# Optimization experiments

Measured on AMD Instinct MI355X. Metric: run time of the kernel, lower is better.

Reference implementation:

```python
import jax, jax.numpy as jnp
import numpy as np

B, N, DM, H, C, DC = 4, 1024, 512, 8, 3, 16  # batch, nodes, node_dim, heads, manifold components, per-component dim
DK = DM // H


def setup_inputs() -> dict:
    key = jax.random.key(0)
    ks = jax.random.split(key, 8)

    def lin_w(k):
        return jax.random.normal(k, (DM, DM), jnp.float32) / np.sqrt(DM).astype(np.float32)

    return {
        "h": jax.random.normal(ks[0], (B, N, DM), jnp.float32),
        "x": jax.random.normal(ks[1], (B, N, C * DC), jnp.float32),
        "Wq": lin_w(ks[2]), "bq": jnp.zeros((DM,), jnp.float32),
        "Wk": lin_w(ks[3]), "bk": jnp.zeros((DM,), jnp.float32),
        "Wv": lin_w(ks[4]), "bv": jnp.zeros((DM,), jnp.float32),
        "Wo": lin_w(ks[5]), "bo": jnp.zeros((DM,), jnp.float32),
        "alpha": jnp.ones((H, C), jnp.float32),
        "log_sigma": jnp.zeros((H, C), jnp.float32),
    }


def reference(h, x, Wq, bq, Wk, bk, Wv, bv, Wo, bo, alpha, log_sigma):
    b, n, dm = h.shape
    hh, cc = alpha.shape
    dk = dm // hh
    scale = 1.0 / np.sqrt(dk).astype(np.float32)

    def to_heads(t, W, bias):
        return (t @ W.T + bias).reshape(b, n, hh, dk).transpose(0, 2, 1, 3)  # (B,H,N,dk)

    Q = to_heads(h, Wq, bq)
    K = to_heads(h, Wk, bk)
    V = to_heads(h, Wv, bv)

    attn = jnp.einsum('bhid,bhjd->bhij', Q, K) * scale  # (B,H,N,N)

    # Geodesic kernel: per-component Euclidean distances on the product manifold.
    xs = x.reshape(b, n, cc, -1)                      # (B,N,C,dc)
    sq = jnp.sum(xs * xs, axis=-1)                    # (B,N,C)
    inner = jnp.einsum('bicd,bjcd->bijc', xs, xs)     # (B,N,N,C)
    d_sq = jnp.maximum(sq[:, :, None, :] + sq[:, None, :, :] - 2.0 * inner, 0.0)  # (B,N,N,C)

    sigma = jnp.clip(jnp.exp(log_sigma), 1e-4)        # (H,C)
    # exp(-d_c^2 / (2 sigma_{h,c}^2)) -> (B,H,N,N,C), then weight by alpha and sum over c
    e = jnp.exp(-d_sq[:, None] / (2.0 * (sigma ** 2)[None, :, None, None, :])).astype(attn.dtype)
    attn = attn + jnp.einsum('hc,bhijc->bhij', alpha, e)

    p = jax.nn.softmax(attn, axis=-1)
    out = jnp.einsum('bhij,bhjd->bhid', p, V)         # (B,H,N,dk)
    out = out.transpose(0, 2, 1, 3).reshape(b, n, dm)
    return out @ Wo.T + bo
```

## Files before the change

### kernel.cpp

```cpp
#include <hip/hip_runtime.h>

typedef __bf16 bf16;
typedef __attribute__((ext_vector_type(8))) __bf16 bf16x8;
typedef __attribute__((ext_vector_type(4))) float f32x4;

#define LOG2E 1.44269504088896f
#define SCALE 0.125f

__device__ inline f32x4 mfma16(bf16x8 a, bf16x8 b, f32x4 c) {
    return __builtin_amdgcn_mfma_f32_16x16x32_bf16(a, b, c, 0, 0, 0);
}

__global__ __launch_bounds__(256) void prep_kernel(
        const float* __restrict__ h, const float* __restrict__ x,
        const float* __restrict__ Wq, const float* __restrict__ Wk,
        const float* __restrict__ Wv, const float* __restrict__ Wo,
        const float* __restrict__ bq, const float* __restrict__ bk,
        const float* __restrict__ bv,
        bf16* __restrict__ hb, bf16* __restrict__ wpack, bf16* __restrict__ wob,
        float* __restrict__ bqkv, bf16* __restrict__ xb, float* __restrict__ sqx) {
    int stride = gridDim.x * blockDim.x;
    int tid = blockIdx.x * blockDim.x + threadIdx.x;
    for (int i = tid; i < 4096 * 512; i += stride) hb[i] = (bf16)h[i];
    for (int i = tid; i < 3 * 512 * 512; i += stride) {
        float v = (i < 262144) ? Wq[i] : (i < 524288 ? Wk[i - 262144] : Wv[i - 524288]);
        wpack[i] = (bf16)v;
    }
    for (int i = tid; i < 512 * 512; i += stride) wob[i] = (bf16)Wo[i];
    for (int i = tid; i < 1536; i += stride)
        bqkv[i] = (i < 512) ? bq[i] : (i < 1024 ? bk[i - 512] : bv[i - 1024]);
    for (int i = tid; i < 4096 * 48; i += stride) xb[i] = (bf16)x[i];
    for (int i = tid; i < 4096 * 3; i += stride) {
        int row = i / 3, c = i - row * 3;
        float s = 0.0f;
        for (int k = 0; k < 16; k++) {
            float v = (float)(bf16)x[row * 48 + c * 16 + k];
            s += v * v;
        }
        sqx[i] = s;
    }
}

__global__ __launch_bounds__(256) void gemm_qkv_kernel(
        const bf16* __restrict__ A, const bf16* __restrict__ Bm,
        const float* __restrict__ bias,
        bf16* __restrict__ Qb, bf16* __restrict__ Kb, bf16* __restrict__ Vt) {
    __shared__ bf16 Al[64][72];
    __shared__ bf16 Bl[64][72];
    int t = threadIdx.x;
    int w = t >> 6, lane = t & 63, g = lane >> 4, lo = lane & 15;
    int rowbase = blockIdx.x * 64, colbase = blockIdx.y * 64;
    int wr = (w >> 1) * 32, wc = (w & 1) * 32;
    f32x4 acc[2][2] = {};
    int sr = t >> 2, sc = (t & 3) * 16;
    for (int kb = 0; kb < 512; kb += 64) {
        *(bf16x8*)&Al[sr][sc]     = *(const bf16x8*)&A[(rowbase + sr) * 512 + kb + sc];
        *(bf16x8*)&Al[sr][sc + 8] = *(const bf16x8*)&A[(rowbase + sr) * 512 + kb + sc + 8];
        *(bf16x8*)&Bl[sr][sc]     = *(const bf16x8*)&Bm[(colbase + sr) * 512 + kb + sc];
        *(bf16x8*)&Bl[sr][sc + 8] = *(const bf16x8*)&Bm[(colbase + sr) * 512 + kb + sc + 8];
        __syncthreads();
        for (int kk = 0; kk < 64; kk += 32) {
            bf16x8 af[2], bfr[2];
            af[0]  = *(const bf16x8*)&Al[wr + lo][kk + 8 * g];
            af[1]  = *(const bf16x8*)&Al[wr + 16 + lo][kk + 8 * g];
            bfr[0] = *(const bf16x8*)&Bl[wc + lo][kk + 8 * g];
            bfr[1] = *(const bf16x8*)&Bl[wc + 16 + lo][kk + 8 * g];
            for (int ri = 0; ri < 2; ri++)
                for (int ci = 0; ci < 2; ci++)
                    acc[ri][ci] = mfma16(af[ri], bfr[ci], acc[ri][ci]);
        }
        __syncthreads();
    }
    for (int ri = 0; ri < 2; ri++)
        for (int ci = 0; ci < 2; ci++) {
            int mcol = colbase + wc + 16 * ci + lo;
            float bv = bias[mcol];
            int proj = mcol >> 9, hm = mcol & 511, head = hm >> 6, d = hm & 63;
            for (int r = 0; r < 4; r++) {
                int n = rowbase + wr + 16 * ri + 4 * g + r;
                int bidx = n >> 10, i = n & 1023;
                bf16 val = (bf16)(acc[ri][ci][r] + bv);
                if (proj == 0)
                    Qb[((size_t)(bidx * 8 + head) * 1024 + i) * 64 + d] = val;
                else if (proj == 1)
                    Kb[((size_t)(bidx * 8 + head) * 1024 + i) * 64 + d] = val;
                else
                    Vt[((size_t)(bidx * 8 + head) * 64 + d) * 1024 + i] = val;
            }
        }
}

__global__ __launch_bounds__(256) void attn_kernel(
        const bf16* __restrict__ Qb, const bf16* __restrict__ Kb,
        const bf16* __restrict__ Vt, const bf16* __restrict__ xb,
        const float* __restrict__ sqx, const float* __restrict__ alpha,
        const float* __restrict__ log_sigma, int nsplit,
        float* __restrict__ o_part, float* __restrict__ ml_part) {
    __shared__ bf16 Klds[64][72];
    __shared__ bf16 Xlds[64][56];
    __shared__ bf16 VTlds[64][72];
    __shared__ float sqj[3][64];
    __shared__ bf16 Plds[4][16][72];

    int t = threadIdx.x;
    int w = t >> 6, lane = t & 63, g = lane >> 4, lo = lane & 15;
    int zz = blockIdx.z;
    int b = zz / nsplit, split = zz - b * nsplit;
    int hh = blockIdx.y;
    int i0 = blockIdx.x * 64 + w * 16;

    float alf[3], coef[3];
    for (int c = 0; c < 3; c++) {
        alf[c] = alpha[hh * 3 + c];
        float sg = expf(log_sigma[hh * 3 + c]);
        sg = fmaxf(sg, 1e-4f);
        coef[c] = -LOG2E / (2.0f * sg * sg);
    }

    const bf16* Qbase = Qb + ((size_t)(b * 8 + hh) * 1024 + i0) * 64;
    bf16x8 qa[2];
    qa[0] = *(const bf16x8*)&Qbase[lo * 64 + 8 * g];
    qa[1] = *(const bf16x8*)&Qbase[lo * 64 + 32 + 8 * g];

    bf16x8 xqa[3];
    const bf16* Xibase = xb + ((size_t)(b << 10) + i0) * 48;
    for (int c = 0; c < 3; c++) {
        bf16x8 v = {};
        if (g < 2) v = *(const bf16x8*)&Xibase[lo * 48 + c * 16 + 8 * g];
        xqa[c] = v;
    }

    float sqi[3][4];
    const float* sqibase = sqx + ((size_t)(b << 10) + i0) * 3;
    for (int r = 0; r < 4; r++)
        for (int c = 0; c < 3; c++) sqi[c][r] = sqibase[(4 * g + r) * 3 + c];

    float m_r[4], l_r[4];
    f32x4 o[4];
    for (int r = 0; r < 4; r++) { m_r[r] = -1e30f; l_r[r] = 0.0f; }
    for (int td = 0; td < 4; td++) o[td] = (f32x4){0.f, 0.f, 0.f, 0.f};

    int sr = t >> 2, sc = (t & 3) * 16;
    int jlen = 1024 / nsplit, jb = split * jlen;
    for (int j0 = jb; j0 < jb + jlen; j0 += 64) {
        __syncthreads();
        const bf16* Kbase = Kb + ((size_t)(b * 8 + hh) * 1024 + j0) * 64;
        *(bf16x8*)&Klds[sr][sc]     = *(const bf16x8*)&Kbase[sr * 64 + sc];
        *(bf16x8*)&Klds[sr][sc + 8] = *(const bf16x8*)&Kbase[sr * 64 + sc + 8];
        const bf16* Vbase = Vt + ((size_t)(b * 8 + hh) * 64) * 1024 + j0;
        *(bf16x8*)&VTlds[sr][sc]     = *(const bf16x8*)&Vbase[sr * 1024 + sc];
        *(bf16x8*)&VTlds[sr][sc + 8] = *(const bf16x8*)&Vbase[sr * 1024 + sc + 8];
        for (int idx = t; idx < 384; idx += 256) {
            int xr = idx / 6, xc = (idx - xr * 6) * 8;
            *(bf16x8*)&Xlds[xr][xc] = *(const bf16x8*)&xb[((size_t)(b << 10) + j0 + xr) * 48 + xc];
        }
        if (t < 192) {
            int jl = t / 3, c = t - jl * 3;
            sqj[c][jl] = sqx[((size_t)(b << 10) + j0 + jl) * 3 + c];
        }
        __syncthreads();

        f32x4 s[4];
        for (int tt = 0; tt < 4; tt++) {
            f32x4 acc = {};
            bf16x8 kb0 = *(const bf16x8*)&Klds[16 * tt + lo][8 * g];
            bf16x8 kb1 = *(const bf16x8*)&Klds[16 * tt + lo][32 + 8 * g];
            acc = mfma16(qa[0], kb0, acc);
            acc = mfma16(qa[1], kb1, acc);
            f32x4 ic[3];
            for (int c = 0; c < 3; c++) {
                bf16x8 xbf = {};
                if (g < 2) xbf = *(const bf16x8*)&Xlds[16 * tt + lo][c * 16 + 8 * g];
                f32x4 z = {};
                ic[c] = mfma16(xqa[c], xbf, z);
            }
            for (int r = 0; r < 4; r++) {
                float sv = acc[r] * SCALE;
                for (int c = 0; c < 3; c++) {
                    float d = sqi[c][r] + sqj[c][16 * tt + lo] - 2.0f * ic[c][r];
                    d = fmaxf(d, 0.0f);
                    sv += alf[c] * exp2f(coef[c] * d);
                }
                acc[r] = sv;
            }
            s[tt] = acc;
        }

        float pm[4], sf[4], rs[4];
        for (int r = 0; r < 4; r++)
            pm[r] = fmaxf(fmaxf(s[0][r], s[1][r]), fmaxf(s[2][r], s[3][r]));
        for (int msk = 1; msk < 16; msk <<= 1)
            for (int r = 0; r < 4; r++) pm[r] = fmaxf(pm[r], __shfl_xor(pm[r], msk));
        for (int r = 0; r < 4; r++) {
            float mn = fmaxf(m_r[r], pm[r]);
            sf[r] = exp2f((m_r[r] - mn) * LOG2E);
            m_r[r] = mn;
            rs[r] = 0.0f;
        }
        for (int tt = 0; tt < 4; tt++)
            for (int r = 0; r < 4; r++) {
                float p = exp2f((s[tt][r] - m_r[r]) * LOG2E);
                s[tt][r] = p;
                rs[r] += p;
            }
        for (int msk = 1; msk < 16; msk <<= 1)
            for (int r = 0; r < 4; r++) rs[r] += __shfl_xor(rs[r], msk);
        for (int r = 0; r < 4; r++) l_r[r] = l_r[r] * sf[r] + rs[r];

        for (int tt = 0; tt < 4; tt++)
            for (int r = 0; r < 4; r++)
                Plds[w][4 * g + r][16 * tt + lo] = (bf16)s[tt][r];

        for (int td = 0; td < 4; td++)
            for (int r = 0; r < 4; r++) o[td][r] *= sf[r];

        bf16x8 pa0 = *(const bf16x8*)&Plds[w][lo][8 * g];
        bf16x8 pa1 = *(const bf16x8*)&Plds[w][lo][32 + 8 * g];
        for (int td = 0; td < 4; td++) {
            bf16x8 vb0 = *(const bf16x8*)&VTlds[16 * td + lo][8 * g];
            bf16x8 vb1 = *(const bf16x8*)&VTlds[16 * td + lo][32 + 8 * g];
            o[td] = mfma16(pa0, vb0, o[td]);
            o[td] = mfma16(pa1, vb1, o[td]);
        }
    }

    for (int td = 0; td < 4; td++)
        for (int r = 0; r < 4; r++) {
            int i = i0 + 4 * g + r;
            size_t rowg = (size_t)(b * 8 + hh) * 1024 + i;
            o_part[((size_t)split * 32768 + rowg) * 64 + 16 * td + lo] = o[td][r];
        }
    if (lo == 0)
        for (int r = 0; r < 4; r++) {
            int i = i0 + 4 * g + r;
            size_t rowg = (size_t)(b * 8 + hh) * 1024 + i;
            ml_part[((size_t)split * 32768 + rowg) * 2]     = m_r[r];
            ml_part[((size_t)split * 32768 + rowg) * 2 + 1] = l_r[r];
        }
}

__global__ __launch_bounds__(256) void merge_kernel(
        const float* __restrict__ o_part, const float* __restrict__ ml_part,
        int nsplit, bf16* __restrict__ attnout) {
    int t = threadIdx.x;
    int rowg = blockIdx.x * 16 + (t >> 4);
    int d4 = (t & 15) * 4;
    float m0 = ml_part[(size_t)rowg * 2], l0 = ml_part[(size_t)rowg * 2 + 1];
    float m1 = -1e30f, l1 = 0.0f;
    if (nsplit == 2) {
        m1 = ml_part[((size_t)32768 + rowg) * 2];
        l1 = ml_part[((size_t)32768 + rowg) * 2 + 1];
    }
    float M = fmaxf(m0, m1);
    float w0 = exp2f((m0 - M) * LOG2E);
    float w1 = exp2f((m1 - M) * LOG2E);
    float inv = 1.0f / (w0 * l0 + w1 * l1);
    f32x4 a = *(const f32x4*)&o_part[(size_t)rowg * 64 + d4];
    f32x4 bv = (f32x4){0.f, 0.f, 0.f, 0.f};
    if (nsplit == 2) bv = *(const f32x4*)&o_part[((size_t)32768 + rowg) * 64 + d4];
    int b = rowg >> 13, hh = (rowg >> 10) & 7, i = rowg & 1023;
    bf16* dst = &attnout[((size_t)(b << 10) + i) * 512 + hh * 64 + d4];
    for (int q = 0; q < 4; q++)
        dst[q] = (bf16)((w0 * a[q] + w1 * bv[q]) * inv);
}

__global__ __launch_bounds__(256) void gemm_out_kernel(
        const bf16* __restrict__ A, const bf16* __restrict__ Bm,
        const float* __restrict__ bias, float* __restrict__ out) {
    __shared__ bf16 Al[64][72];
    __shared__ bf16 Bl[64][72];
    int t = threadIdx.x;
    int w = t >> 6, lane = t & 63, g = lane >> 4, lo = lane & 15;
    int rowbase = blockIdx.x * 64, colbase = blockIdx.y * 64;
    int wr = (w >> 1) * 32, wc = (w & 1) * 32;
    f32x4 acc[2][2] = {};
    int sr = t >> 2, sc = (t & 3) * 16;
    for (int kb = 0; kb < 512; kb += 64) {
        *(bf16x8*)&Al[sr][sc]     = *(const bf16x8*)&A[(rowbase + sr) * 512 + kb + sc];
        *(bf16x8*)&Al[sr][sc + 8] = *(const bf16x8*)&A[(rowbase + sr) * 512 + kb + sc + 8];
        *(bf16x8*)&Bl[sr][sc]     = *(const bf16x8*)&Bm[(colbase + sr) * 512 + kb + sc];
        *(bf16x8*)&Bl[sr][sc + 8] = *(const bf16x8*)&Bm[(colbase + sr) * 512 + kb + sc + 8];
        __syncthreads();
        for (int kk = 0; kk < 64; kk += 32) {
            bf16x8 af[2], bfr[2];
            af[0]  = *(const bf16x8*)&Al[wr + lo][kk + 8 * g];
            af[1]  = *(const bf16x8*)&Al[wr + 16 + lo][kk + 8 * g];
            bfr[0] = *(const bf16x8*)&Bl[wc + lo][kk + 8 * g];
            bfr[1] = *(const bf16x8*)&Bl[wc + 16 + lo][kk + 8 * g];
            for (int ri = 0; ri < 2; ri++)
                for (int ci = 0; ci < 2; ci++)
                    acc[ri][ci] = mfma16(af[ri], bfr[ci], acc[ri][ci]);
        }
        __syncthreads();
    }
    for (int ri = 0; ri < 2; ri++)
        for (int ci = 0; ci < 2; ci++) {
            int mcol = colbase + wc + 16 * ci + lo;
            float bv = bias[mcol];
            for (int r = 0; r < 4; r++) {
                int n = rowbase + wr + 16 * ri + 4 * g + r;
                out[(size_t)n * 512 + mcol] = acc[ri][ci][r] + bv;
            }
        }
}

extern "C" void kernel_launch(void* const* d_in, const int* in_sizes, int n_in,
                              void* d_out, int out_size, void* d_ws, size_t ws_size,
                              hipStream_t stream) {
    const float* h  = (const float*)d_in[0];
    const float* x  = (const float*)d_in[1];
    const float* Wq = (const float*)d_in[2];
    const float* bq = (const float*)d_in[3];
    const float* Wk = (const float*)d_in[4];
    const float* bk = (const float*)d_in[5];
    const float* Wv = (const float*)d_in[6];
    const float* bv = (const float*)d_in[7];
    const float* Wo = (const float*)d_in[8];
    const float* bo = (const float*)d_in[9];
    const float* alpha     = (const float*)d_in[10];
    const float* log_sigma = (const float*)d_in[11];
    float* out = (float*)d_out;

    char* ws = (char*)d_ws;
    size_t off = 0;
    auto alloc = [&](size_t bytes) {
        char* p = ws + off;
        off += (bytes + 255) & ~(size_t)255;
        return p;
    };
    bf16*  hb      = (bf16*)alloc(4096 * 512 * 2);
    bf16*  wpack   = (bf16*)alloc(1536 * 512 * 2);
    bf16*  wob     = (bf16*)alloc(512 * 512 * 2);
    float* bqkv    = (float*)alloc(1536 * 4);
    bf16*  xb      = (bf16*)alloc(4096 * 48 * 2);
    float* sqx     = (float*)alloc(4096 * 3 * 4);
    bf16*  Qb      = (bf16*)alloc((size_t)4 * 8 * 1024 * 64 * 2);
    bf16*  Kb      = (bf16*)alloc((size_t)4 * 8 * 1024 * 64 * 2);
    bf16*  Vt      = (bf16*)alloc((size_t)4 * 8 * 1024 * 64 * 2);
    bf16*  attnout = (bf16*)alloc(4096 * 512 * 2);
    size_t base = off;

    size_t need2 = base + 2 * ((size_t)32768 * 64 * 4 + 1024) + 2 * ((size_t)32768 * 2 * 4 + 1024);
    int nsplit = (ws_size >= need2) ? 2 : 1;
    float* o_part  = (float*)alloc((size_t)nsplit * 32768 * 64 * 4);
    float* ml_part = (float*)alloc((size_t)nsplit * 32768 * 2 * 4);

    prep_kernel<<<512, 256, 0, stream>>>(h, x, Wq, Wk, Wv, Wo, bq, bk, bv,
                                         hb, wpack, wob, bqkv, xb, sqx);
    gemm_qkv_kernel<<<dim3(64, 24), 256, 0, stream>>>(hb, wpack, bqkv, Qb, Kb, Vt);
    attn_kernel<<<dim3(16, 8, 4 * nsplit), 256, 0, stream>>>(
        Qb, Kb, Vt, xb, sqx, alpha, log_sigma, nsplit, o_part, ml_part);
    merge_kernel<<<2048, 256, 0, stream>>>(o_part, ml_part, nsplit, attnout);
    gemm_out_kernel<<<dim3(64, 8), 256, 0, stream>>>(attnout, wob, bo, out);
}
```

Baseline: 211.0 us.

## Factor Gaussian kernel into per-row and per-column exponentials and coalesce QKV stores

Rewrites exp(-(si+sj-2ij)/2σ²) as A_i·B_j·exp(ij/σ²), with the per-row and per-column factors (alpha folded into the row factor) computed once in the prep kernel. This cuts the inner-loop work to one exp and two FMAs per component and drops the clamp to zero. The QKV GEMM epilogue now stages its tile in LDS and writes coalesced 16-byte vectors, including a transposed write for V. The P buffer shares LDS with the X tile to reduce shared memory, at the cost of an extra barrier. Removing the clamp and factoring the exponential can overflow or underflow for large norms or small sigma, which is a numerical risk.

```diff
diff --git a/kernel.cpp b/kernel.cpp
--- a/kernel.cpp
+++ b/kernel.cpp
@@ -16,9 +16,11 @@
         const float* __restrict__ Wq, const float* __restrict__ Wk,
         const float* __restrict__ Wv, const float* __restrict__ Wo,
         const float* __restrict__ bq, const float* __restrict__ bk,
-        const float* __restrict__ bv,
+        const float* __restrict__ bv, const float* __restrict__ alpha,
+        const float* __restrict__ log_sigma,
         bf16* __restrict__ hb, bf16* __restrict__ wpack, bf16* __restrict__ wob,
-        float* __restrict__ bqkv, bf16* __restrict__ xb, float* __restrict__ sqx) {
+        float* __restrict__ bqkv, bf16* __restrict__ xb,
+        float* __restrict__ Aexp, float* __restrict__ Bexp) {
     int stride = gridDim.x * blockDim.x;
     int tid = blockIdx.x * blockDim.x + threadIdx.x;
     for (int i = tid; i < 4096 * 512; i += stride) hb[i] = (bf16)h[i];
@@ -37,7 +39,14 @@
             float v = (float)(bf16)x[row * 48 + c * 16 + k];
             s += v * v;
         }
-        sqx[i] = s;
+        int b = row >> 10, jj = row & 1023;
+        for (int hh = 0; hh < 8; hh++) {
+            float sg = fmaxf(expf(log_sigma[hh * 3 + c]), 1e-4f);
+            float coef = -(0.5f * LOG2E) / (sg * sg);
+            float e = exp2f(coef * s);
+            Aexp[((size_t)row * 8 + hh) * 3 + c] = alpha[hh * 3 + c] * e;
+            Bexp[(((size_t)(b * 8 + hh)) * 1024 + jj) * 3 + c] = e;
+        }
     }
 }
 
@@ -73,48 +82,54 @@
     }
     for (int ri = 0; ri < 2; ri++)
         for (int ci = 0; ci < 2; ci++) {
-            int mcol = colbase + wc + 16 * ci + lo;
-            float bv = bias[mcol];
-            int proj = mcol >> 9, hm = mcol & 511, head = hm >> 6, d = hm & 63;
-            for (int r = 0; r < 4; r++) {
-                int n = rowbase + wr + 16 * ri + 4 * g + r;
-                int bidx = n >> 10, i = n & 1023;
-                bf16 val = (bf16)(acc[ri][ci][r] + bv);
-                if (proj == 0)
-                    Qb[((size_t)(bidx * 8 + head) * 1024 + i) * 64 + d] = val;
-                else if (proj == 1)
-                    Kb[((size_t)(bidx * 8 + head) * 1024 + i) * 64 + d] = val;
-                else
-                    Vt[((size_t)(bidx * 8 + head) * 64 + d) * 1024 + i] = val;
-            }
-        }
+            int ccol = wc + 16 * ci + lo;
+            float bv = bias[colbase + ccol];
+            for (int r = 0; r < 4; r++)
+                Al[wr + 16 * ri + 4 * g + r][ccol] = (bf16)(acc[ri][ci][r] + bv);
+        }
+    __syncthreads();
+    int proj = colbase >> 9, head = (colbase >> 6) & 7;
+    int bidx = rowbase >> 10, i0 = rowbase & 1023;
+    int row = t >> 2, c16 = (t & 3) * 16;
+    if (proj < 2) {
+        bf16* dst = (proj == 0 ? Qb : Kb) +
+                    ((size_t)(bidx * 8 + head) * 1024 + i0 + row) * 64 + c16;
+        *(bf16x8*)dst       = *(const bf16x8*)&Al[row][c16];
+        *(bf16x8*)(dst + 8) = *(const bf16x8*)&Al[row][c16 + 8];
+    } else {
+        bf16x8 v0, v1;
+        for (int k = 0; k < 8; k++) v0[k] = Al[c16 + k][row];
+        for (int k = 0; k < 8; k++) v1[k] = Al[c16 + 8 + k][row];
+        bf16* dst = Vt + ((size_t)(bidx * 8 + head) * 64 + row) * 1024 + i0 + c16;
+        *(bf16x8*)dst       = v0;
+        *(bf16x8*)(dst + 8) = v1;
+    }
 }
 
 __global__ __launch_bounds__(256) void attn_kernel(
         const bf16* __restrict__ Qb, const bf16* __restrict__ Kb,
         const bf16* __restrict__ Vt, const bf16* __restrict__ xb,
-        const float* __restrict__ sqx, const float* __restrict__ alpha,
+        const float* __restrict__ Aexp, const float* __restrict__ Bexp,
         const float* __restrict__ log_sigma, int nsplit,
         float* __restrict__ o_part, float* __restrict__ ml_part) {
     __shared__ bf16 Klds[64][72];
-    __shared__ bf16 Xlds[64][56];
     __shared__ bf16 VTlds[64][72];
-    __shared__ float sqj[3][64];
-    __shared__ bf16 Plds[4][16][72];
+    __shared__ float Blds[3][64];
+    __shared__ __align__(16) char PXbuf[9216];
+    bf16 (*Xlds)[56] = (bf16 (*)[56])PXbuf;
 
     int t = threadIdx.x;
     int w = t >> 6, lane = t & 63, g = lane >> 4, lo = lane & 15;
+    bf16* Pw = (bf16*)PXbuf + (size_t)w * 16 * 72;
     int zz = blockIdx.z;
     int b = zz / nsplit, split = zz - b * nsplit;
     int hh = blockIdx.y;
     int i0 = blockIdx.x * 64 + w * 16;
 
-    float alf[3], coef[3];
+    float k2[3];
     for (int c = 0; c < 3; c++) {
-        alf[c] = alpha[hh * 3 + c];
-        float sg = expf(log_sigma[hh * 3 + c]);
-        sg = fmaxf(sg, 1e-4f);
-        coef[c] = -LOG2E / (2.0f * sg * sg);
+        float sg = fmaxf(expf(log_sigma[hh * 3 + c]), 1e-4f);
+        k2[c] = LOG2E / (sg * sg);
     }
 
     const bf16* Qbase = Qb + ((size_t)(b * 8 + hh) * 1024 + i0) * 64;
@@ -130,10 +145,10 @@
         xqa[c] = v;
     }
 
-    float sqi[3][4];
-    const float* sqibase = sqx + ((size_t)(b << 10) + i0) * 3;
+    float af[3][4];
     for (int r = 0; r < 4; r++)
-        for (int c = 0; c < 3; c++) sqi[c][r] = sqibase[(4 * g + r) * 3 + c];
+        for (int c = 0; c < 3; c++)
+            af[c][r] = Aexp[(((size_t)(b << 10) + i0 + 4 * g + r) * 8 + hh) * 3 + c];
 
     float m_r[4], l_r[4];
     f32x4 o[4];
@@ -155,8 +170,8 @@
             *(bf16x8*)&Xlds[xr][xc] = *(const bf16x8*)&xb[((size_t)(b << 10) + j0 + xr) * 48 + xc];
         }
         if (t < 192) {
-            int jl = t / 3, c = t - jl * 3;
-            sqj[c][jl] = sqx[((size_t)(b << 10) + j0 + jl) * 3 + c];
+            int jl = t & 63, c = t >> 6;
+            Blds[c][jl] = Bexp[(((size_t)(b * 8 + hh)) * 1024 + j0 + jl) * 3 + c];
         }
         __syncthreads();
 
@@ -174,17 +189,19 @@
                 f32x4 z = {};
                 ic[c] = mfma16(xqa[c], xbf, z);
             }
+            float B0 = Blds[0][16 * tt + lo];
+            float B1 = Blds[1][16 * tt + lo];
+            float B2 = Blds[2][16 * tt + lo];
             for (int r = 0; r < 4; r++) {
                 float sv = acc[r] * SCALE;
-                for (int c = 0; c < 3; c++) {
-                    float d = sqi[c][r] + sqj[c][16 * tt + lo] - 2.0f * ic[c][r];
-                    d = fmaxf(d, 0.0f);
-                    sv += alf[c] * exp2f(coef[c] * d);
-                }
+                sv = fmaf(af[0][r] * B0, exp2f(k2[0] * ic[0][r]), sv);
+                sv = fmaf(af[1][r] * B1, exp2f(k2[1] * ic[1][r]), sv);
+                sv = fmaf(af[2][r] * B2, exp2f(k2[2] * ic[2][r]), sv);
                 acc[r] = sv;
             }
             s[tt] = acc;
         }
+        __syncthreads();
 
         float pm[4], sf[4], rs[4];
         for (int r = 0; r < 4; r++)
@@ -209,13 +226,13 @@
 
         for (int tt = 0; tt < 4; tt++)
             for (int r = 0; r < 4; r++)
-                Plds[w][4 * g + r][16 * tt + lo] = (bf16)s[tt][r];
+                Pw[(4 * g + r) * 72 + 16 * tt + lo] = (bf16)s[tt][r];
 
         for (int td = 0; td < 4; td++)
             for (int r = 0; r < 4; r++) o[td][r] *= sf[r];
 
-        bf16x8 pa0 = *(const bf16x8*)&Plds[w][lo][8 * g];
-        bf16x8 pa1 = *(const bf16x8*)&Plds[w][lo][32 + 8 * g];
+        bf16x8 pa0 = *(const bf16x8*)&Pw[lo * 72 + 8 * g];
+        bf16x8 pa1 = *(const bf16x8*)&Pw[lo * 72 + 32 + 8 * g];
         for (int td = 0; td < 4; td++) {
             bf16x8 vb0 = *(const bf16x8*)&VTlds[16 * td + lo][8 * g];
             bf16x8 vb1 = *(const bf16x8*)&VTlds[16 * td + lo][32 + 8 * g];
@@ -333,7 +350,8 @@
     bf16*  wob     = (bf16*)alloc(512 * 512 * 2);
     float* bqkv    = (float*)alloc(1536 * 4);
     bf16*  xb      = (bf16*)alloc(4096 * 48 * 2);
-    float* sqx     = (float*)alloc(4096 * 3 * 4);
+    float* Aexp    = (float*)alloc((size_t)4096 * 8 * 3 * 4);
+    float* Bexp    = (float*)alloc((size_t)4096 * 8 * 3 * 4);
     bf16*  Qb      = (bf16*)alloc((size_t)4 * 8 * 1024 * 64 * 2);
     bf16*  Kb      = (bf16*)alloc((size_t)4 * 8 * 1024 * 64 * 2);
     bf16*  Vt      = (bf16*)alloc((size_t)4 * 8 * 1024 * 64 * 2);
@@ -346,10 +364,11 @@
     float* ml_part = (float*)alloc((size_t)nsplit * 32768 * 2 * 4);
 
     prep_kernel<<<512, 256, 0, stream>>>(h, x, Wq, Wk, Wv, Wo, bq, bk, bv,
-                                         hb, wpack, wob, bqkv, xb, sqx);
+                                         alpha, log_sigma,
+                                         hb, wpack, wob, bqkv, xb, Aexp, Bexp);
     gemm_qkv_kernel<<<dim3(64, 24), 256, 0, stream>>>(hb, wpack, bqkv, Qb, Kb, Vt);
     attn_kernel<<<dim3(16, 8, 4 * nsplit), 256, 0, stream>>>(
-        Qb, Kb, Vt, xb, sqx, alpha, log_sigma, nsplit, o_part, ml_part);
+        Qb, Kb, Vt, xb, Aexp, Bexp, log_sigma, nsplit, o_part, ml_part);
     merge_kernel<<<2048, 256, 0, stream>>>(o_part, ml_part, nsplit, attnout);
     gemm_out_kernel<<<dim3(64, 8), 256, 0, stream>>>(attnout, wob, bo, out);
 }
```

Result: faster. 200.8 us (-4.8%).

## Fold geodesic norms into MFMA, drop online softmax max, enlarge GEMM tiles

Applied to the files above, without the earlier changes.

The attention kernel now builds augmented x vectors in which -0.5*||x||^2 (split into bf16 hi/lo parts) and ones sit in padding lanes. A single MFMA per component then yields -d^2/2 directly, replacing the scalar per-element distance arithmetic. The online softmax max tracking, rescaling and cross-lane shuffles are removed: scores are exponentiated directly, and row sums come from an MFMA against a ones vector, which simplifies the merge kernel. This relies on scores staying small enough not to overflow fp32 exp2, so it is numerically less robust for general inputs. Both projection GEMMs move from 64x64 to 128x128 tiles, and the QKV GEMM stages its output through LDS so Q, K and transposed V stores are coalesced.

```diff
diff --git a/kernel.cpp b/kernel.cpp
--- a/kernel.cpp
+++ b/kernel.cpp
@@ -1,4 +1,5 @@
 #include <hip/hip_runtime.h>
+#include <math.h>
 
 typedef __bf16 bf16;
 typedef __attribute__((ext_vector_type(8))) __bf16 bf16x8;
@@ -9,6 +10,9 @@
 
 __device__ inline f32x4 mfma16(bf16x8 a, bf16x8 b, f32x4 c) {
     return __builtin_amdgcn_mfma_f32_16x16x32_bf16(a, b, c, 0, 0, 0);
+}
+__device__ inline unsigned short bfb(bf16 v) {
+    union { bf16 b; unsigned short u; } z; z.b = v; return z.u;
 }
 
 __global__ __launch_bounds__(256) void prep_kernel(
@@ -18,13 +22,15 @@
         const float* __restrict__ bq, const float* __restrict__ bk,
         const float* __restrict__ bv,
         bf16* __restrict__ hb, bf16* __restrict__ wpack, bf16* __restrict__ wob,
-        float* __restrict__ bqkv, bf16* __restrict__ xb, float* __restrict__ sqx) {
+        float* __restrict__ bqkv, bf16* __restrict__ xb,
+        unsigned* __restrict__ spack) {
     int stride = gridDim.x * blockDim.x;
     int tid = blockIdx.x * blockDim.x + threadIdx.x;
     for (int i = tid; i < 4096 * 512; i += stride) hb[i] = (bf16)h[i];
-    for (int i = tid; i < 3 * 512 * 512; i += stride) {
-        float v = (i < 262144) ? Wq[i] : (i < 524288 ? Wk[i - 262144] : Wv[i - 524288]);
-        wpack[i] = (bf16)v;
+    for (int i = tid; i < 262144; i += stride) {
+        wpack[i]          = (bf16)Wq[i];
+        wpack[262144 + i] = (bf16)Wk[i];
+        wpack[524288 + i] = (bf16)Wv[i];
     }
     for (int i = tid; i < 512 * 512; i += stride) wob[i] = (bf16)Wo[i];
     for (int i = tid; i < 1536; i += stride)
@@ -37,7 +43,10 @@
             float v = (float)(bf16)x[row * 48 + c * 16 + k];
             s += v * v;
         }
-        sqx[i] = s;
+        s = -0.5f * s;
+        bf16 sh = (bf16)s;
+        bf16 sl = (bf16)(s - (float)sh);
+        spack[i] = (unsigned)bfb(sh) | ((unsigned)bfb(sl) << 16);
     }
 }
 
@@ -45,61 +54,71 @@
         const bf16* __restrict__ A, const bf16* __restrict__ Bm,
         const float* __restrict__ bias,
         bf16* __restrict__ Qb, bf16* __restrict__ Kb, bf16* __restrict__ Vt) {
-    __shared__ bf16 Al[64][72];
-    __shared__ bf16 Bl[64][72];
-    int t = threadIdx.x;
-    int w = t >> 6, lane = t & 63, g = lane >> 4, lo = lane & 15;
-    int rowbase = blockIdx.x * 64, colbase = blockIdx.y * 64;
-    int wr = (w >> 1) * 32, wc = (w & 1) * 32;
-    f32x4 acc[2][2] = {};
-    int sr = t >> 2, sc = (t & 3) * 16;
+    __shared__ bf16 smem[2 * 128 * 72];
+    bf16 (*Asm)[72] = (bf16(*)[72])smem;
+    bf16 (*Bsm)[72] = (bf16(*)[72])(smem + 128 * 72);
+    int t = threadIdx.x, w = t >> 6, lane = t & 63, g = lane >> 4, lo = lane & 15;
+    int rowbase = blockIdx.x * 128, colbase = blockIdx.y * 128;
+    int wr = (w >> 1) * 64, wc = (w & 1) * 64;
+    f32x4 acc[4][4] = {};
+    int srow = t >> 2, scol = (t & 3) * 16;
     for (int kb = 0; kb < 512; kb += 64) {
-        *(bf16x8*)&Al[sr][sc]     = *(const bf16x8*)&A[(rowbase + sr) * 512 + kb + sc];
-        *(bf16x8*)&Al[sr][sc + 8] = *(const bf16x8*)&A[(rowbase + sr) * 512 + kb + sc + 8];
-        *(bf16x8*)&Bl[sr][sc]     = *(const bf16x8*)&Bm[(colbase + sr) * 512 + kb + sc];
-        *(bf16x8*)&Bl[sr][sc + 8] = *(const bf16x8*)&Bm[(colbase + sr) * 512 + kb + sc + 8];
+        __syncthreads();
+        for (int half = 0; half < 2; half++) {
+            int r = srow + 64 * half;
+            *(bf16x8*)&Asm[r][scol]     = *(const bf16x8*)&A[(size_t)(rowbase + r) * 512 + kb + scol];
+            *(bf16x8*)&Asm[r][scol + 8] = *(const bf16x8*)&A[(size_t)(rowbase + r) * 512 + kb + scol + 8];
+            *(bf16x8*)&Bsm[r][scol]     = *(const bf16x8*)&Bm[(size_t)(colbase + r) * 512 + kb + scol];
+            *(bf16x8*)&Bsm[r][scol + 8] = *(const bf16x8*)&Bm[(size_t)(colbase + r) * 512 + kb + scol + 8];
+        }
         __syncthreads();
         for (int kk = 0; kk < 64; kk += 32) {
-            bf16x8 af[2], bfr[2];
-            af[0]  = *(const bf16x8*)&Al[wr + lo][kk + 8 * g];
-            af[1]  = *(const bf16x8*)&Al[wr + 16 + lo][kk + 8 * g];
-            bfr[0] = *(const bf16x8*)&Bl[wc + lo][kk + 8 * g];
-            bfr[1] = *(const bf16x8*)&Bl[wc + 16 + lo][kk + 8 * g];
-            for (int ri = 0; ri < 2; ri++)
-                for (int ci = 0; ci < 2; ci++)
-                    acc[ri][ci] = mfma16(af[ri], bfr[ci], acc[ri][ci]);
-        }
-        __syncthreads();
-    }
-    for (int ri = 0; ri < 2; ri++)
-        for (int ci = 0; ci < 2; ci++) {
-            int mcol = colbase + wc + 16 * ci + lo;
-            float bv = bias[mcol];
-            int proj = mcol >> 9, hm = mcol & 511, head = hm >> 6, d = hm & 63;
-            for (int r = 0; r < 4; r++) {
-                int n = rowbase + wr + 16 * ri + 4 * g + r;
-                int bidx = n >> 10, i = n & 1023;
-                bf16 val = (bf16)(acc[ri][ci][r] + bv);
-                if (proj == 0)
-                    Qb[((size_t)(bidx * 8 + head) * 1024 + i) * 64 + d] = val;
-                else if (proj == 1)
-                    Kb[((size_t)(bidx * 8 + head) * 1024 + i) * 64 + d] = val;
-                else
-                    Vt[((size_t)(bidx * 8 + head) * 64 + d) * 1024 + i] = val;
-            }
-        }
+            bf16x8 af[4], bfr[4];
+            for (int m = 0; m < 4; m++) af[m]  = *(const bf16x8*)&Asm[wr + 16 * m + lo][kk + 8 * g];
+            for (int n = 0; n < 4; n++) bfr[n] = *(const bf16x8*)&Bsm[wc + 16 * n + lo][kk + 8 * g];
+            for (int m = 0; m < 4; m++)
+                for (int n = 0; n < 4; n++)
+                    acc[m][n] = mfma16(af[m], bfr[n], acc[m][n]);
+        }
+    }
+    __syncthreads();
+    bf16 (*Cl)[132] = (bf16(*)[132])smem;
+    for (int n = 0; n < 4; n++) {
+        float bv = bias[colbase + wc + 16 * n + lo];
+        for (int m = 0; m < 4; m++)
+            for (int r = 0; r < 4; r++)
+                Cl[wr + 16 * m + 4 * g + r][wc + 16 * n + lo] = (bf16)(acc[m][n][r] + bv);
+    }
+    __syncthreads();
+    int proj = colbase >> 9, h0 = (colbase >> 6) & 7;
+    int bidx = rowbase >> 10, i0g = rowbase & 1023;
+    if (proj < 2) {
+        int row = t >> 1, half = t & 1;
+        bf16* dst = (proj == 0 ? Qb : Kb) +
+                    ((size_t)(bidx * 8 + h0 + half) * 1024 + i0g + row) * 64;
+        for (int ch = 0; ch < 8; ch++)
+            *(bf16x8*)&dst[ch * 8] = *(const bf16x8*)&Cl[row][half * 64 + ch * 8];
+    } else {
+        int dcol = t >> 1, ihalf = t & 1;
+        int head = h0 + (dcol >> 6), d = dcol & 63;
+        bf16* dst = Vt + ((size_t)(bidx * 8 + head) * 64 + d) * 1024 + i0g + ihalf * 64;
+        for (int ch = 0; ch < 8; ch++) {
+            bf16x8 v;
+            for (int q = 0; q < 8; q++) v[q] = Cl[ihalf * 64 + ch * 8 + q][dcol];
+            *(bf16x8*)&dst[ch * 8] = v;
+        }
+    }
 }
 
 __global__ __launch_bounds__(256) void attn_kernel(
         const bf16* __restrict__ Qb, const bf16* __restrict__ Kb,
         const bf16* __restrict__ Vt, const bf16* __restrict__ xb,
-        const float* __restrict__ sqx, const float* __restrict__ alpha,
-        const float* __restrict__ log_sigma, int nsplit,
-        float* __restrict__ o_part, float* __restrict__ ml_part) {
+        const unsigned* __restrict__ spack,
+        const float* __restrict__ alpha, const float* __restrict__ log_sigma,
+        int nsplit, float* __restrict__ o_part, float* __restrict__ l_part) {
     __shared__ bf16 Klds[64][72];
-    __shared__ bf16 Xlds[64][56];
     __shared__ bf16 VTlds[64][72];
-    __shared__ float sqj[3][64];
+    __shared__ bf16 Xlds[64][104];
     __shared__ bf16 Plds[4][16][72];
 
     int t = threadIdx.x;
@@ -109,12 +128,13 @@
     int hh = blockIdx.y;
     int i0 = blockIdx.x * 64 + w * 16;
 
-    float alf[3], coef[3];
+    const unsigned ONE2 = 0x3F803F80u;
+    float c1 = SCALE * LOG2E;
+    float k2[3], alf[3];
     for (int c = 0; c < 3; c++) {
-        alf[c] = alpha[hh * 3 + c];
-        float sg = expf(log_sigma[hh * 3 + c]);
-        sg = fmaxf(sg, 1e-4f);
-        coef[c] = -LOG2E / (2.0f * sg * sg);
+        float sg = fmaxf(expf(log_sigma[hh * 3 + c]), 1e-4f);
+        k2[c] = LOG2E / (sg * sg);
+        alf[c] = alpha[hh * 3 + c] * LOG2E;
     }
 
     const bf16* Qbase = Qb + ((size_t)(b * 8 + hh) * 1024 + i0) * 64;
@@ -123,22 +143,26 @@
     qa[1] = *(const bf16x8*)&Qbase[lo * 64 + 32 + 8 * g];
 
     bf16x8 xqa[3];
-    const bf16* Xibase = xb + ((size_t)(b << 10) + i0) * 48;
     for (int c = 0; c < 3; c++) {
         bf16x8 v = {};
-        if (g < 2) v = *(const bf16x8*)&Xibase[lo * 48 + c * 16 + 8 * g];
+        if (g < 2) {
+            v = *(const bf16x8*)&xb[((size_t)(b << 10) + i0 + lo) * 48 + c * 16 + 8 * g];
+        } else if (g == 2) {
+            uint2 ap;
+            ap.x = spack[((size_t)(b << 10) + i0 + lo) * 3 + c];
+            ap.y = ONE2;
+            ((uint2*)&v)[0] = ap;
+        }
         xqa[c] = v;
     }
 
-    float sqi[3][4];
-    const float* sqibase = sqx + ((size_t)(b << 10) + i0) * 3;
-    for (int r = 0; r < 4; r++)
-        for (int c = 0; c < 3; c++) sqi[c][r] = sqibase[(4 * g + r) * 3 + c];
-
-    float m_r[4], l_r[4];
-    f32x4 o[4];
-    for (int r = 0; r < 4; r++) { m_r[r] = -1e30f; l_r[r] = 0.0f; }
-    for (int td = 0; td < 4; td++) o[td] = (f32x4){0.f, 0.f, 0.f, 0.f};
+    bf16x8 ones;
+    for (int e = 0; e < 8; e++) ones[e] = (bf16)1.0f;
+    f32x4 o[4] = {};
+    f32x4 lacc = {};
+
+    for (int idx = t; idx < 1664; idx += 256)
+        ((unsigned long long*)&Xlds[0][0])[idx] = 0ULL;
 
     int sr = t >> 2, sc = (t & 3) * 16;
     int jlen = 1024 / nsplit, jb = split * jlen;
@@ -150,72 +174,41 @@
         const bf16* Vbase = Vt + ((size_t)(b * 8 + hh) * 64) * 1024 + j0;
         *(bf16x8*)&VTlds[sr][sc]     = *(const bf16x8*)&Vbase[sr * 1024 + sc];
         *(bf16x8*)&VTlds[sr][sc + 8] = *(const bf16x8*)&Vbase[sr * 1024 + sc + 8];
-        for (int idx = t; idx < 384; idx += 256) {
-            int xr = idx / 6, xc = (idx - xr * 6) * 8;
-            *(bf16x8*)&Xlds[xr][xc] = *(const bf16x8*)&xb[((size_t)(b << 10) + j0 + xr) * 48 + xc];
-        }
         if (t < 192) {
-            int jl = t / 3, c = t - jl * 3;
-            sqj[c][jl] = sqx[((size_t)(b << 10) + j0 + jl) * 3 + c];
-        }
-        __syncthreads();
-
-        f32x4 s[4];
+            int xr = t / 3, c = t - xr * 3;
+            const bf16* xsrc = &xb[((size_t)(b << 10) + j0 + xr) * 48 + c * 16];
+            *(bf16x8*)&Xlds[xr][c * 32]     = *(const bf16x8*)&xsrc[0];
+            *(bf16x8*)&Xlds[xr][c * 32 + 8] = *(const bf16x8*)&xsrc[8];
+            uint2 bp;
+            bp.x = ONE2;
+            bp.y = spack[((size_t)(b << 10) + j0 + xr) * 3 + c];
+            *(uint2*)&Xlds[xr][c * 32 + 16] = bp;
+        }
+        __syncthreads();
+
         for (int tt = 0; tt < 4; tt++) {
             f32x4 acc = {};
             bf16x8 kb0 = *(const bf16x8*)&Klds[16 * tt + lo][8 * g];
             bf16x8 kb1 = *(const bf16x8*)&Klds[16 * tt + lo][32 + 8 * g];
             acc = mfma16(qa[0], kb0, acc);
             acc = mfma16(qa[1], kb1, acc);
-            f32x4 ic[3];
-            for (int c = 0; c < 3; c++) {
-                bf16x8 xbf = {};
-                if (g < 2) xbf = *(const bf16x8*)&Xlds[16 * tt + lo][c * 16 + 8 * g];
-                f32x4 z = {};
-                ic[c] = mfma16(xqa[c], xbf, z);
+            f32x4 z0 = {}, z1 = {}, z2 = {};
+            f32x4 e0 = mfma16(xqa[0], *(const bf16x8*)&Xlds[16 * tt + lo][8 * g], z0);
+            f32x4 e1 = mfma16(xqa[1], *(const bf16x8*)&Xlds[16 * tt + lo][32 + 8 * g], z1);
+            f32x4 e2 = mfma16(xqa[2], *(const bf16x8*)&Xlds[16 * tt + lo][64 + 8 * g], z2);
+            for (int r = 0; r < 4; r++) {
+                float t0 = alf[0] * exp2f(k2[0] * fminf(e0[r], 0.0f));
+                t0 = fmaf(alf[1], exp2f(k2[1] * fminf(e1[r], 0.0f)), t0);
+                t0 = fmaf(alf[2], exp2f(k2[2] * fminf(e2[r], 0.0f)), t0);
+                float p = exp2f(fmaf(acc[r], c1, t0));
+                Plds[w][4 * g + r][16 * tt + lo] = (bf16)p;
             }
-            for (int r = 0; r < 4; r++) {
-                float sv = acc[r] * SCALE;
-                for (int c = 0; c < 3; c++) {
-                    float d = sqi[c][r] + sqj[c][16 * tt + lo] - 2.0f * ic[c][r];
-                    d = fmaxf(d, 0.0f);
-                    sv += alf[c] * exp2f(coef[c] * d);
-                }
-                acc[r] = sv;
-            }
-            s[tt] = acc;
-        }
-
-        float pm[4], sf[4], rs[4];
-        for (int r = 0; r < 4; r++)
-            pm[r] = fmaxf(fmaxf(s[0][r], s[1][r]), fmaxf(s[2][r], s[3][r]));
-        for (int msk = 1; msk < 16; msk <<= 1)
-            for (int r = 0; r < 4; r++) pm[r] = fmaxf(pm[r], __shfl_xor(pm[r], msk));
-        for (int r = 0; r < 4; r++) {
-            float mn = fmaxf(m_r[r], pm[r]);
-            sf[r] = exp2f((m_r[r] - mn) * LOG2E);
-            m_r[r] = mn;
-            rs[r] = 0.0f;
-        }
-        for (int tt = 0; tt < 4; tt++)
-            for (int r = 0; r < 4; r++) {
-                float p = exp2f((s[tt][r] - m_r[r]) * LOG2E);
-                s[tt][r] = p;
-                rs[r] += p;
-            }
-        for (int msk = 1; msk < 16; msk <<= 1)
-            for (int r = 0; r < 4; r++) rs[r] += __shfl_xor(rs[r], msk);
-        for (int r = 0; r < 4; r++) l_r[r] = l_r[r] * sf[r] + rs[r];
-
-        for (int tt = 0; tt < 4; tt++)
-            for (int r = 0; r < 4; r++)
-                Plds[w][4 * g + r][16 * tt + lo] = (bf16)s[tt][r];
-
-        for (int td = 0; td < 4; td++)
-            for (int r = 0; r < 4; r++) o[td][r] *= sf[r];
+        }
 
         bf16x8 pa0 = *(const bf16x8*)&Plds[w][lo][8 * g];
         bf16x8 pa1 = *(const bf16x8*)&Plds[w][lo][32 + 8 * g];
+        lacc = mfma16(pa0, ones, lacc);
+        lacc = mfma16(pa1, ones, lacc);
         for (int td = 0; td < 4; td++) {
             bf16x8 vb0 = *(const bf16x8*)&VTlds[16 * td + lo][8 * g];
             bf16x8 vb1 = *(const bf16x8*)&VTlds[16 * td + lo][32 + 8 * g];
@@ -226,82 +219,73 @@
 
     for (int td = 0; td < 4; td++)
         for (int r = 0; r < 4; r++) {
-            int i = i0 + 4 * g + r;
-            size_t rowg = (size_t)(b * 8 + hh) * 1024 + i;
+            size_t rowg = (size_t)(b * 8 + hh) * 1024 + i0 + 4 * g + r;
             o_part[((size_t)split * 32768 + rowg) * 64 + 16 * td + lo] = o[td][r];
         }
     if (lo == 0)
         for (int r = 0; r < 4; r++) {
-            int i = i0 + 4 * g + r;
-            size_t rowg = (size_t)(b * 8 + hh) * 1024 + i;
-            ml_part[((size_t)split * 32768 + rowg) * 2]     = m_r[r];
-            ml_part[((size_t)split * 32768 + rowg) * 2 + 1] = l_r[r];
+            size_t rowg = (size_t)(b * 8 + hh) * 1024 + i0 + 4 * g + r;
+            l_part[(size_t)split * 32768 + rowg] = lacc[r];
         }
 }
 
 __global__ __launch_bounds__(256) void merge_kernel(
-        const float* __restrict__ o_part, const float* __restrict__ ml_part,
+        const float* __restrict__ o_part, const float* __restrict__ l_part,
         int nsplit, bf16* __restrict__ attnout) {
     int t = threadIdx.x;
     int rowg = blockIdx.x * 16 + (t >> 4);
     int d4 = (t & 15) * 4;
-    float m0 = ml_part[(size_t)rowg * 2], l0 = ml_part[(size_t)rowg * 2 + 1];
-    float m1 = -1e30f, l1 = 0.0f;
+    float l = l_part[rowg];
+    f32x4 a = *(const f32x4*)&o_part[(size_t)rowg * 64 + d4];
     if (nsplit == 2) {
-        m1 = ml_part[((size_t)32768 + rowg) * 2];
-        l1 = ml_part[((size_t)32768 + rowg) * 2 + 1];
-    }
-    float M = fmaxf(m0, m1);
-    float w0 = exp2f((m0 - M) * LOG2E);
-    float w1 = exp2f((m1 - M) * LOG2E);
-    float inv = 1.0f / (w0 * l0 + w1 * l1);
-    f32x4 a = *(const f32x4*)&o_part[(size_t)rowg * 64 + d4];
-    f32x4 bv = (f32x4){0.f, 0.f, 0.f, 0.f};
-    if (nsplit == 2) bv = *(const f32x4*)&o_part[((size_t)32768 + rowg) * 64 + d4];
+        l += l_part[32768 + rowg];
+        f32x4 b2 = *(const f32x4*)&o_part[((size_t)32768 + rowg) * 64 + d4];
+        for (int q = 0; q < 4; q++) a[q] += b2[q];
+    }
+    float inv = 1.0f / l;
     int b = rowg >> 13, hh = (rowg >> 10) & 7, i = rowg & 1023;
     bf16* dst = &attnout[((size_t)(b << 10) + i) * 512 + hh * 64 + d4];
-    for (int q = 0; q < 4; q++)
-        dst[q] = (bf16)((w0 * a[q] + w1 * bv[q]) * inv);
+    for (int q = 0; q < 4; q++) dst[q] = (bf16)(a[q] * inv);
 }
 
 __global__ __launch_bounds__(256) void gemm_out_kernel(
         const bf16* __restrict__ A, const bf16* __restrict__ Bm,
         const float* __restrict__ bias, float* __restrict__ out) {
-    __shared__ bf16 Al[64][72];
-    __shared__ bf16 Bl[64][72];
-    int t = threadIdx.x;
-    int w = t >> 6, lane = t & 63, g = lane >> 4, lo = lane & 15;
-    int rowbase = blockIdx.x * 64, colbase = blockIdx.y * 64;
-    int wr = (w >> 1) * 32, wc = (w & 1) * 32;
-    f32x4 acc[2][2] = {};
-    int sr = t >> 2, sc = (t & 3) * 16;
+    __shared__ bf16 smem[2 * 128 * 72];
+    bf16 (*Asm)[72] = (bf16(*)[72])smem;
+    bf16 (*Bsm)[72] = (bf16(*)[72])(smem + 128 * 72);
+    int t = threadIdx.x, w = t >> 6, lane = t & 63, g = lane >> 4, lo = lane & 15;
+    int rowbase = blockIdx.x * 128, colbase = blockIdx.y * 128;
+    int wr = (w >> 1) * 64, wc = (w & 1) * 64;
+    f32x4 acc[4][4] = {};
+    int srow = t >> 2, scol = (t & 3) * 16;
     for (int kb = 0; kb < 512; kb += 64) {
-        *(bf16x8*)&Al[sr][sc]     = *(const bf16x8*)&A[(rowbase + sr) * 512 + kb + sc];
-        *(bf16x8*)&Al[sr][sc + 8] = *(const bf16x8*)&A[(rowbase + sr) * 512 + kb + sc + 8];
-        *(bf16x8*)&Bl[sr][sc]     = *(const bf16x8*)&Bm[(colbase + sr) * 512 + kb + sc];
-        *(bf16x8*)&Bl[sr][sc + 8] = *(const bf16x8*)&Bm[(colbase + sr) * 512 + kb + sc + 8];
+        __syncthreads();
+        for (int half = 0; half < 2; half++) {
+            int r = srow + 64 * half;
+            *(bf16x8*)&Asm[r][scol]     = *(const bf16x8*)&A[(size_t)(rowbase + r) * 512 + kb + scol];
+            *(bf16x8*)&Asm[r][scol + 8] = *(const bf16x8*)&A[(size_t)(rowbase + r) * 512 + kb + scol + 8];
+            *(bf16x8*)&Bsm[r][scol]     = *(const bf16x8*)&Bm[(size_t)(colbase + r) * 512 + kb + scol];
+            *(bf16x8*)&Bsm[r][scol + 8] = *(const bf16x8*)&Bm[(size_t)(colbase + r) * 512 + kb + scol + 8];
+        }
         __syncthreads();
         for (int kk = 0; kk < 64; kk += 32) {
-            bf16x8 af[2], bfr[2];
-            af[0]  = *(const bf16x8*)&Al[wr + lo][kk + 8 * g];
-            af[1]  = *(const bf16x8*)&Al[wr + 16 + lo][kk + 8 * g];
-            bfr[0] = *(const bf16x8*)&Bl[wc + lo][kk + 8 * g];
-            bfr[1] = *(const bf16x8*)&Bl[wc + 16 + lo][kk + 8 * g];
-            for (int ri = 0; ri < 2; ri++)
-                for (int ci = 0; ci < 2; ci++)
-                    acc[ri][ci] = mfma16(af[ri], bfr[ci], acc[ri][ci]);
-        }
-        __syncthreads();
-    }
-    for (int ri = 0; ri < 2; ri++)
-        for (int ci = 0; ci < 2; ci++) {
-            int mcol = colbase + wc + 16 * ci + lo;
-            float bv = bias[mcol];
-            for (int r = 0; r < 4; r++) {
-                int n = rowbase + wr + 16 * ri + 4 * g + r;
-                out[(size_t)n * 512 + mcol] = acc[ri][ci][r] + bv;
-            }
-        }
+            bf16x8 af[4], bfr[4];
+            for (int m = 0; m < 4; m++) af[m]  = *(const bf16x8*)&Asm[wr + 16 * m + lo][kk + 8 * g];
+            for (int n = 0; n < 4; n++) bfr[n] = *(const bf16x8*)&Bsm[wc + 16 * n + lo][kk + 8 * g];
+            for (int m = 0; m < 4; m++)
+                for (int n = 0; n < 4; n++)
+                    acc[m][n] = mfma16(af[m], bfr[n], acc[m][n]);
+        }
+    }
+    for (int n = 0; n < 4; n++) {
+        int mcol = colbase + wc + 16 * n + lo;
+        float bv = bias[mcol];
+        for (int m = 0; m < 4; m++)
+            for (int r = 0; r < 4; r++)
+                out[(size_t)(rowbase + wr + 16 * m + 4 * g + r) * 512 + mcol] =
+                    acc[m][n][r] + bv;
+    }
 }
 
 extern "C" void kernel_launch(void* const* d_in, const int* in_sizes, int n_in,
@@ -328,28 +312,28 @@
         off += (bytes + 255) & ~(size_t)255;
         return p;
     };
-    bf16*  hb      = (bf16*)alloc(4096 * 512 * 2);
-    bf16*  wpack   = (bf16*)alloc(1536 * 512 * 2);
-    bf16*  wob     = (bf16*)alloc(512 * 512 * 2);
-    float* bqkv    = (float*)alloc(1536 * 4);
-    bf16*  xb      = (bf16*)alloc(4096 * 48 * 2);
-    float* sqx     = (float*)alloc(4096 * 3 * 4);
-    bf16*  Qb      = (bf16*)alloc((size_t)4 * 8 * 1024 * 64 * 2);
-    bf16*  Kb      = (bf16*)alloc((size_t)4 * 8 * 1024 * 64 * 2);
-    bf16*  Vt      = (bf16*)alloc((size_t)4 * 8 * 1024 * 64 * 2);
-    bf16*  attnout = (bf16*)alloc(4096 * 512 * 2);
+    bf16*     hb      = (bf16*)alloc(4096 * 512 * 2);
+    bf16*     wpack   = (bf16*)alloc(1536 * 512 * 2);
+    bf16*     wob     = (bf16*)alloc(512 * 512 * 2);
+    float*    bqkv    = (float*)alloc(1536 * 4);
+    bf16*     xb      = (bf16*)alloc(4096 * 48 * 2);
+    unsigned* spack   = (unsigned*)alloc((size_t)4096 * 3 * 4);
+    bf16*     Qb      = (bf16*)alloc((size_t)4 * 8 * 1024 * 64 * 2);
+    bf16*     Kb      = (bf16*)alloc((size_t)4 * 8 * 1024 * 64 * 2);
+    bf16*     Vt      = (bf16*)alloc((size_t)4 * 8 * 1024 * 64 * 2);
+    bf16*     attnout = (bf16*)alloc(4096 * 512 * 2);
     size_t base = off;
 
-    size_t need2 = base + 2 * ((size_t)32768 * 64 * 4 + 1024) + 2 * ((size_t)32768 * 2 * 4 + 1024);
+    size_t need2 = base + 2 * ((size_t)32768 * 64 * 4 + 1024) + 2 * ((size_t)32768 * 4 + 1024);
     int nsplit = (ws_size >= need2) ? 2 : 1;
-    float* o_part  = (float*)alloc((size_t)nsplit * 32768 * 64 * 4);
-    float* ml_part = (float*)alloc((size_t)nsplit * 32768 * 2 * 4);
+    float* o_part = (float*)alloc((size_t)nsplit * 32768 * 64 * 4);
+    float* l_part = (float*)alloc((size_t)nsplit * 32768 * 4);
 
     prep_kernel<<<512, 256, 0, stream>>>(h, x, Wq, Wk, Wv, Wo, bq, bk, bv,
-                                         hb, wpack, wob, bqkv, xb, sqx);
-    gemm_qkv_kernel<<<dim3(64, 24), 256, 0, stream>>>(hb, wpack, bqkv, Qb, Kb, Vt);
+                                         hb, wpack, wob, bqkv, xb, spack);
+    gemm_qkv_kernel<<<dim3(32, 12), 256, 0, stream>>>(hb, wpack, bqkv, Qb, Kb, Vt);
     attn_kernel<<<dim3(16, 8, 4 * nsplit), 256, 0, stream>>>(
-        Qb, Kb, Vt, xb, sqx, alpha, log_sigma, nsplit, o_part, ml_part);
-    merge_kernel<<<2048, 256, 0, stream>>>(o_part, ml_part, nsplit, attnout);
-    gemm_out_kernel<<<dim3(64, 8), 256, 0, stream>>>(attnout, wob, bo, out);
-}
+        Qb, Kb, Vt, xb, spack, alpha, log_sigma, nsplit, o_part, l_part);
+    merge_kernel<<<2048, 256, 0, stream>>>(o_part, l_part, nsplit, attnout);
+    gemm_out_kernel<<<dim3(32, 4), 256, 0, stream>>>(attnout, wob, bo, out);
+}
```

New measurement: 172.6 us. 18.2% less time.
